# Optimization experiments

Hardware: AMD Instinct MI355X
Metric: run time of the kernel (lower is better)

The kernel has to match this reference:

```python
import jax, jax.numpy as jnp
import numpy as np

B, N, DIM = 2, 2048, 1024
H, DH = 16, 64
INNER = H * DH
LN_EPS = 1e-5
ATTN_EPS = 1e-8
SCALE = DH ** -0.5


def setup_inputs() -> dict:
    key = jax.random.key(0)
    k1, k2, k3 = jax.random.split(key, 3)
    x = jax.random.normal(k1, (B, N, DIM), dtype=jnp.float32)
    ln_gamma = jnp.ones((DIM,), dtype=jnp.float32)
    ln_beta = jnp.zeros((DIM,), dtype=jnp.float32)
    w_qkv = jax.random.normal(k2, (DIM, 3 * INNER), dtype=jnp.float32) * 0.02
    w_out = jax.random.normal(k3, (INNER, DIM), dtype=jnp.float32) * 0.02
    b_out = jnp.zeros((DIM,), dtype=jnp.float32)
    return {"x": x, "ln_gamma": ln_gamma, "ln_beta": ln_beta,
            "w_qkv": w_qkv, "w_out": w_out, "b_out": b_out}


def reference(x, ln_gamma, ln_beta, w_qkv, w_out, b_out):
    # LayerNorm over last dim (biased variance, eps=1e-5)
    mu = jnp.mean(x, axis=-1, keepdims=True)
    var = jnp.var(x, axis=-1, keepdims=True)
    xn = (x - mu) * jax.lax.rsqrt(var + LN_EPS) * ln_gamma + ln_beta
    # QKV projection (no bias), split heads: b n (h d) -> b h n d
    qkv = xn @ w_qkv                                    # [B, N, 3*INNER]
    q, k, v = jnp.split(qkv, 3, axis=-1)
    split_heads = lambda t: t.reshape(B, N, H, DH).transpose(0, 2, 1, 3)
    q, k, v = split_heads(q), split_heads(k), split_heads(v)
    # 'softmax' attn_type: exp(scale * q k^T), normalized by row-sum + eps
    scores = jnp.einsum('bhnd,bhmd->bhnm', q, k) * SCALE   # [B, H, N, N]
    numer = jnp.exp(scores)
    denom = jnp.sum(numer, axis=-1, keepdims=True) + ATTN_EPS
    attn = numer / denom
    out = jnp.einsum('bhnm,bhmd->bhnd', attn, v)           # [B, H, N, DH]
    out = out.transpose(0, 2, 1, 3).reshape(B, N, INNER)   # b h n d -> b n (h d)
    return out @ w_out + b_out
```

## Files before the change

### kernel.cpp

```cpp
#include <hip/hip_runtime.h>
#include <hip/hip_bf16.h>

#define NB    2
#define SEQ   2048
#define DIM_  1024
#define NH    16
#define DHD   64
#define INNER 1024
#define ROWS  4096

typedef _Float16 half_t;
typedef __attribute__((ext_vector_type(4))) _Float16 half4;
typedef __attribute__((ext_vector_type(8))) _Float16 half8;
typedef __attribute__((ext_vector_type(4))) float f32x4;
typedef __attribute__((ext_vector_type(16))) float f32x16;
typedef __attribute__((ext_vector_type(2))) int int2v;
typedef __attribute__((ext_vector_type(4))) int int4v;

__device__ __forceinline__ void async16(const void* g, void* l) {
    __builtin_amdgcn_global_load_lds(
        (const __attribute__((address_space(1))) unsigned int*)g,
        (__attribute__((address_space(3))) unsigned int*)l, 16, 0, 0);
}

__device__ __forceinline__ float ldf(const void* p, size_t i, int isb) {
    if (isb) {
        unsigned int v = ((unsigned int)((const unsigned short*)p)[i]) << 16;
        return __uint_as_float(v);
    }
    return ((const float*)p)[i];
}

__global__ void detect_dtype(const unsigned short* x, int* flag) {
    int tid = threadIdx.x;
    int cnt = 0;
    for (int i = tid; i < 2048; i += 64) {
        float f = __uint_as_float(((unsigned int)x[2 * i]) << 16);
        float a = fabsf(f);
        if (a >= 0.0009765625f && a <= 16.0f) cnt++;
    }
    for (int off = 32; off > 0; off >>= 1) cnt += __shfl_down(cnt, off);
    if (tid == 0) flag[0] = (cnt > 1024) ? 1 : 0;
}

__global__ __launch_bounds__(256) void ln_kernel(const void* __restrict__ x,
                                                 const void* __restrict__ gamma,
                                                 const void* __restrict__ beta,
                                                 half_t* __restrict__ xn,
                                                 const int* __restrict__ flag) {
    int row = blockIdx.x;
    int isb = flag[0];
    int tid = threadIdx.x;
    float vals[4];
    float s = 0.f, ss = 0.f;
    if (!isb) {
        float4 xv = *(const float4*)((const float*)x + (size_t)row * DIM_ + tid * 4);
        vals[0] = xv.x; vals[1] = xv.y; vals[2] = xv.z; vals[3] = xv.w;
    } else {
        #pragma unroll
        for (int j = 0; j < 4; j++) vals[j] = ldf(x, (size_t)row * DIM_ + tid * 4 + j, isb);
    }
    #pragma unroll
    for (int j = 0; j < 4; j++) { s += vals[j]; ss += vals[j] * vals[j]; }
    __shared__ float red[2][4];
    for (int off = 32; off > 0; off >>= 1) {
        s += __shfl_down(s, off);
        ss += __shfl_down(ss, off);
    }
    int wid = tid >> 6;
    if ((tid & 63) == 0) { red[0][wid] = s; red[1][wid] = ss; }
    __syncthreads();
    if (tid == 0) {
        float S = 0.f, SS = 0.f;
        for (int w = 0; w < 4; w++) { S += red[0][w]; SS += red[1][w]; }
        float mu = S / 1024.f;
        float var = SS / 1024.f - mu * mu;
        red[0][0] = mu;
        red[1][0] = rsqrtf(var + 1e-5f);
    }
    __syncthreads();
    float mu = red[0][0], r = red[1][0];
    half4 o;
    #pragma unroll
    for (int j = 0; j < 4; j++) {
        int c = tid * 4 + j;
        float g = ldf(gamma, c, isb);
        float b = ldf(beta, c, isb);
        o[j] = (half_t)((vals[j] - mu) * r * g + b);
    }
    *(half4*)(xn + (size_t)row * DIM_ + tid * 4) = o;
}

__global__ __launch_bounds__(256) void wtrans(const void* __restrict__ W,
                                              half_t* __restrict__ WT,
                                              int K_, int N_,
                                              const int* __restrict__ flag) {
    __shared__ half_t T[64][72];
    int isb = flag[0];
    int k0 = blockIdx.y * 64, n0 = blockIdx.x * 64;
    int t = threadIdx.x;
    if (!isb) {
        #pragma unroll
        for (int p = 0; p < 4; p++) {
            int idx = p * 256 + t;
            int r = idx >> 4, c4 = (idx & 15) * 4;
            float4 xv = *(const float4*)((const float*)W + (size_t)(k0 + r) * N_ + n0 + c4);
            T[r][c4] = (half_t)xv.x; T[r][c4 + 1] = (half_t)xv.y;
            T[r][c4 + 2] = (half_t)xv.z; T[r][c4 + 3] = (half_t)xv.w;
        }
    } else {
        int c = t & 63, rw = t >> 6;
        #pragma unroll
        for (int p = 0; p < 16; p++) {
            int r = p * 4 + rw;
            T[r][c] = (half_t)ldf(W, (size_t)(k0 + r) * N_ + n0 + c, isb);
        }
    }
    __syncthreads();
    int c = t & 63, rw = t >> 6;
    #pragma unroll
    for (int p = 0; p < 16; p++) {
        int r = p * 4 + rw;
        WT[(size_t)(n0 + r) * K_ + k0 + c] = T[c][r];
    }
}

__global__ __launch_bounds__(256) void qkv_gemm(const half_t* __restrict__ A,
                                                const half_t* __restrict__ BT,
                                                half_t* __restrict__ q,
                                                half_t* __restrict__ kp,
                                                half_t* __restrict__ vp) {
    __shared__ half_t As[128 * 64];
    __shared__ half_t Bs[128 * 64];
    int t = threadIdx.x;
    int w = t >> 6, l = t & 63;
    int lm = l & 15, q4 = l >> 4;
    int bid = blockIdx.y * 24 + blockIdx.x;
    int xcd = bid & 7, jj = bid >> 3;
    int r0 = (xcd * 4 + jj / 24) * 128, c0 = (jj % 24) * 128;
    int wr = (w >> 1) * 64, wc = (w & 1) * 64;
    int srow = l >> 3, sg = l & 7;
    f32x4 acc[4][4] = {};
    for (int k0 = 0; k0 < 1024; k0 += 64) {
        __syncthreads();
        #pragma unroll
        for (int p = 0; p < 4; p++) {
            int row = p * 32 + w * 8 + srow;
            int g = sg ^ (srow & 7);
            async16(A + (size_t)(r0 + row) * 1024 + k0 + g * 8, &As[(p * 32 + w * 8) * 64]);
            async16(BT + (size_t)(c0 + row) * 1024 + k0 + g * 8, &Bs[(p * 32 + w * 8) * 64]);
        }
        __syncthreads();
        #pragma unroll
        for (int s = 0; s < 2; s++) {
            half8 av[4], bv[4];
            #pragma unroll
            for (int i = 0; i < 4; i++) {
                int gp = ((s * 4 + q4) ^ (lm & 7)) * 8;
                av[i] = *(const half8*)&As[(wr + i * 16 + lm) * 64 + gp];
                bv[i] = *(const half8*)&Bs[(wc + i * 16 + lm) * 64 + gp];
            }
            #pragma unroll
            for (int i = 0; i < 4; i++)
                #pragma unroll
                for (int j = 0; j < 4; j++)
                    acc[i][j] = __builtin_amdgcn_mfma_f32_16x16x32_f16(bv[j], av[i], acc[i][j], 0, 0, 0);
        }
    }
    #pragma unroll
    for (int i = 0; i < 4; i++) {
        int row = r0 + wr + i * 16 + lm;
        int bb = row >> 11, nn = row & 2047;
        #pragma unroll
        for (int j = 0; j < 4; j++) {
            int f0 = c0 + wc + j * 16 + q4 * 4;
            int which = f0 >> 10, within = f0 & 1023;
            int h = within >> 6, d0 = within & 63;
            int bh = bb * NH + h;
            if (which == 0) {
                half4 val;
                #pragma unroll
                for (int r = 0; r < 4; r++) val[r] = (half_t)acc[i][j][r];
                *(half4*)&q[((size_t)bh * SEQ + nn) * DHD + d0] = val;
            } else if (which == 1) {
                int kt = nn >> 7, kb = (nn >> 5) & 3, qi = nn & 31;
                int ks = d0 >> 4, hf = (d0 >> 3) & 1, e = d0 & 7;
                half4 val;
                #pragma unroll
                for (int r = 0; r < 4; r++) val[r] = (half_t)acc[i][j][r];
                size_t off = ((size_t)bh * 16 + kt) * 8192 +
                             (size_t)(((kb * 4 + ks) * 2 + hf) * 32 + qi) * 8 + e;
                *(half4*)&kp[off] = val;
            } else {
                int kt = nn >> 7, k_in = nn & 127;
                int kb = k_in >> 5, c2 = (k_in >> 4) & 1, rem = k_in & 15;
                int hfv = (rem >> 2) & 1, ev = (rem & 3) | ((rem >> 3) << 2);
                size_t bkt = ((size_t)bh * 16 + kt) * 8192;
                #pragma unroll
                for (int r = 0; r < 4; r++) {
                    int d = d0 + r;
                    int mt2 = d >> 5, qi = d & 31;
                    size_t off = bkt +
                        (size_t)((((kb * 2 + c2) * 2 + mt2) * 64 + hfv * 32 + qi) * 8 + ev);
                    vp[off] = (half_t)acc[i][j][r];
                }
            }
        }
    }
}

__global__ __launch_bounds__(256) void out_gemm(const half_t* __restrict__ A,
                                                const half_t* __restrict__ BT,
                                                const void* __restrict__ bias,
                                                void* __restrict__ outp,
                                                const int* __restrict__ flag) {
    __shared__ half_t As[64 * 64];
    __shared__ half_t Bs[128 * 64];
    int isb = flag[0];
    int t = threadIdx.x;
    int w = t >> 6, l = t & 63;
    int lm = l & 15, q4 = l >> 4;
    int bid = blockIdx.y * 8 + blockIdx.x;
    int xcd = bid & 7, jj = bid >> 3;
    int r0 = (xcd * 8 + jj / 8) * 64, c0 = (jj % 8) * 128;
    int wr = (w >> 1) * 32, wc = (w & 1) * 64;
    int srow = l >> 3, sg = l & 7;
    f32x4 acc[2][4] = {};
    for (int k0 = 0; k0 < 1024; k0 += 64) {
        __syncthreads();
        #pragma unroll
        for (int p = 0; p < 2; p++) {
            int row = p * 32 + w * 8 + srow;
            int g = sg ^ (srow & 7);
            async16(A + (size_t)(r0 + row) * 1024 + k0 + g * 8, &As[(p * 32 + w * 8) * 64]);
        }
        #pragma unroll
        for (int p = 0; p < 4; p++) {
            int row = p * 32 + w * 8 + srow;
            int g = sg ^ (srow & 7);
            async16(BT + (size_t)(c0 + row) * 1024 + k0 + g * 8, &Bs[(p * 32 + w * 8) * 64]);
        }
        __syncthreads();
        #pragma unroll
        for (int s = 0; s < 2; s++) {
            int gp = ((s * 4 + q4) ^ (lm & 7)) * 8;
            half8 av[2], bv[4];
            #pragma unroll
            for (int i = 0; i < 2; i++)
                av[i] = *(const half8*)&As[(wr + i * 16 + lm) * 64 + gp];
            #pragma unroll
            for (int j = 0; j < 4; j++)
                bv[j] = *(const half8*)&Bs[(wc + j * 16 + lm) * 64 + gp];
            #pragma unroll
            for (int i = 0; i < 2; i++)
                #pragma unroll
                for (int j = 0; j < 4; j++)
                    acc[i][j] = __builtin_amdgcn_mfma_f32_16x16x32_f16(bv[j], av[i], acc[i][j], 0, 0, 0);
        }
    }
    #pragma unroll
    for (int i = 0; i < 2; i++) {
        int row = r0 + wr + i * 16 + lm;
        #pragma unroll
        for (int j = 0; j < 4; j++) {
            int col0 = c0 + wc + j * 16 + q4 * 4;
            if (!isb) {
                float4 val;
                float* vpp = (float*)&val;
                #pragma unroll
                for (int r = 0; r < 4; r++)
                    vpp[r] = acc[i][j][r] + ((const float*)bias)[col0 + r];
                *(float4*)&((float*)outp)[(size_t)row * DIM_ + col0] = val;
            } else {
                #pragma unroll
                for (int r = 0; r < 4; r++) {
                    float val = acc[i][j][r] + ldf(bias, col0 + r, isb);
                    ((__hip_bfloat16*)outp)[(size_t)row * DIM_ + col0 + r] = __float2bfloat16(val);
                }
            }
        }
    }
}

__global__ __launch_bounds__(512, 4) void attn_mfma(const half_t* __restrict__ q,
                                                    const half_t* __restrict__ kp,
                                                    const half_t* __restrict__ vp,
                                                    half_t* __restrict__ ao) {
    __shared__ __align__(16) char smem[66048];
    int t = threadIdx.x;
    int w = t >> 6, l = t & 63;
    int qi = l & 31, hf = l >> 5;
    int wq = w & 3, wk = w >> 2;
    int bid = blockIdx.x;
    int xcd = bid & 7, jj = bid >> 3;
    int bh = xcd * 4 + (jj >> 4), qt = jj & 15;
    int b = bh >> 4, hd = bh & 15;
    int qrow = qt * 128 + wq * 32 + qi;

    const char* kpb = (const char*)kp + (size_t)bh * 16 * 16384;
    const char* vpb = (const char*)vp + (size_t)bh * 16 * 16384;

    half8 qf[4];
    #pragma unroll
    for (int ks = 0; ks < 4; ks++) {
        qf[ks] = *(const half8*)(q + ((size_t)bh * SEQ + qrow) * DHD + ks * 16 + hf * 8);
        qf[ks] *= (_Float16)0.125f;
    }

    f32x16 oacc[2] = {};
    float lacc = 0.f;

    #pragma unroll
    for (int r = 0; r < 2; r++) {
        async16(kpb + r * 8192 + w * 1024 + l * 16, smem + r * 8192 + w * 1024);
        async16(vpb + r * 8192 + w * 1024 + l * 16, smem + 16384 + r * 8192 + w * 1024);
    }

    for (int kt = 0; kt < 16; kt++) {
        int cur = kt & 1;
        __syncthreads();
        if (kt < 15) {
            const char* kg = kpb + (size_t)(kt + 1) * 16384;
            const char* vg = vpb + (size_t)(kt + 1) * 16384;
            char* dst = smem + (cur ^ 1) * 32768;
            #pragma unroll
            for (int r = 0; r < 2; r++) {
                async16(kg + r * 8192 + w * 1024 + l * 16, dst + r * 8192 + w * 1024);
                async16(vg + r * 8192 + w * 1024 + l * 16, dst + 16384 + r * 8192 + w * 1024);
            }
        }
        const half_t* Kt = (const half_t*)(smem + cur * 32768);
        const half_t* Vt = (const half_t*)(smem + cur * 32768 + 16384);
        half8 kreg[2][4];
        #pragma unroll
        for (int mt = 0; mt < 2; mt++)
            #pragma unroll
            for (int ks = 0; ks < 4; ks++)
                kreg[mt][ks] = *(const half8*)(Kt + ((wk * 2 + mt) * 4 + ks) * 512 + l * 8);
        half8 vreg[2][2][2];
        #pragma unroll
        for (int mt = 0; mt < 2; mt++)
            #pragma unroll
            for (int c = 0; c < 2; c++)
                #pragma unroll
                for (int mt2 = 0; mt2 < 2; mt2++)
                    vreg[mt][c][mt2] = *(const half8*)(Vt +
                        (((wk * 2 + mt) * 2 + c) * 2 + mt2) * 512 + l * 8);
        #pragma unroll
        for (int mt = 0; mt < 2; mt++) {
            f32x16 sacc = {};
            #pragma unroll
            for (int ks = 0; ks < 4; ks++)
                sacc = __builtin_amdgcn_mfma_f32_32x32x16_f16(kreg[mt][ks], qf[ks], sacc, 0, 0, 0);
            half4 quads[4];
            #pragma unroll
            for (int g = 0; g < 4; g++) {
                #pragma unroll
                for (int s2 = 0; s2 < 4; s2++) {
                    float e = __expf(sacc[g * 4 + s2]);
                    lacc += e;
                    quads[g][s2] = (half_t)e;
                }
            }
            #pragma unroll
            for (int c = 0; c < 2; c++) {
                int2v s0 = __builtin_bit_cast(int2v, quads[2 * c]);
                int2v s1 = __builtin_bit_cast(int2v, quads[2 * c + 1]);
                int4v bi;
                bi.x = s0.x; bi.y = s0.y; bi.z = s1.x; bi.w = s1.y;
                half8 bfrag = __builtin_bit_cast(half8, bi);
                #pragma unroll
                for (int mt2 = 0; mt2 < 2; mt2++)
                    oacc[mt2] = __builtin_amdgcn_mfma_f32_32x32x16_f16(vreg[mt][c][mt2], bfrag, oacc[mt2], 0, 0, 0);
            }
        }
    }
    lacc += __shfl_xor(lacc, 32);

    float* Osh = (float*)smem;
    float* Lsh = (float*)(smem + 65536);
    if (wk == 1) {
        #pragma unroll
        for (int mt2 = 0; mt2 < 2; mt2++)
            #pragma unroll
            for (int reg = 0; reg < 16; reg++) {
                int d = mt2 * 32 + (reg & 3) + 8 * (reg >> 2) + 4 * hf;
                Osh[wq * 2048 + d * 32 + qi] = oacc[mt2][reg];
            }
        if (hf == 0) Lsh[wq * 32 + qi] = lacc;
    }
    __syncthreads();
    if (wk == 0) {
        float ltot = lacc + Lsh[wq * 32 + qi];
        float inv = 1.0f / (ltot + 1e-8f);
        #pragma unroll
        for (int mt2 = 0; mt2 < 2; mt2++)
            #pragma unroll
            for (int r2 = 0; r2 < 4; r2++) {
                int d0 = mt2 * 32 + 8 * r2 + 4 * hf;
                half4 ov;
                #pragma unroll
                for (int r = 0; r < 4; r++) {
                    float vsum = oacc[mt2][r2 * 4 + r] + Osh[wq * 2048 + (d0 + r) * 32 + qi];
                    ov[r] = (_Float16)(vsum * inv);
                }
                *(half4*)(ao + (size_t)(b * SEQ + qrow) * INNER + hd * 64 + d0) = ov;
            }
    }
}

extern "C" void kernel_launch(void* const* d_in, const int* in_sizes, int n_in,
                              void* d_out, int out_size, void* d_ws, size_t ws_size,
                              hipStream_t stream) {
    const void* x     = d_in[0];
    const void* gamma = d_in[1];
    const void* beta  = d_in[2];
    const void* wqkv  = d_in[3];
    const void* wout  = d_in[4];
    const void* bout  = d_in[5];

    char* ws = (char*)d_ws;
    int*    flag   = (int*)ws;
    half_t* xn16   = (half_t*)(ws + 256);
    half_t* wqkvT  = xn16  + (size_t)4096 * 1024;
    half_t* woutT  = wqkvT + (size_t)3072 * 1024;
    half_t* q16    = woutT + (size_t)1024 * 1024;
    half_t* kp16   = q16   + (size_t)4096 * 1024;
    half_t* vp16   = kp16  + (size_t)4096 * 1024;
    half_t* ao16   = vp16  + (size_t)4096 * 1024;

    detect_dtype<<<1, 64, 0, stream>>>((const unsigned short*)x, flag);
    ln_kernel<<<ROWS, 256, 0, stream>>>(x, gamma, beta, xn16, flag);
    wtrans<<<dim3(48, 16), 256, 0, stream>>>(wqkv, wqkvT, 1024, 3072, flag);
    wtrans<<<dim3(16, 16), 256, 0, stream>>>(wout, woutT, 1024, 1024, flag);
    qkv_gemm<<<dim3(24, 32), 256, 0, stream>>>(xn16, wqkvT, q16, kp16, vp16);
    attn_mfma<<<dim3(512), 512, 0, stream>>>(q16, kp16, vp16, ao16);
    out_gemm<<<dim3(8, 64), 256, 0, stream>>>(ao16, woutT, bout, d_out, flag);
}
```

Baseline: 207.3 us.

## Process two query subtiles per warp to reuse K/V fragments in attention

Each attention block now covers 256 query rows instead of 128, and each warp handles two 32-row query subtiles. This lets the K and V fragments loaded from LDS feed twice as many MFMAs, and the grid is halved to 256 blocks. The aim is to cut LDS and global K/V traffic per query row. In exchange register pressure rises (the occupancy hint in launch bounds is dropped), there are fewer blocks to hide latency, and an extra barrier is needed because the output reduction buffer now covers the whole of shared memory.

Result: faster. 202.8 us (-2.2%).

```diff
diff --git a/kernel.cpp b/kernel.cpp
--- a/kernel.cpp
+++ b/kernel.cpp
@@ -282,33 +282,36 @@
     }
 }
 
-__global__ __launch_bounds__(512, 4) void attn_mfma(const half_t* __restrict__ q,
-                                                    const half_t* __restrict__ kp,
-                                                    const half_t* __restrict__ vp,
-                                                    half_t* __restrict__ ao) {
-    __shared__ __align__(16) char smem[66048];
+__global__ __launch_bounds__(512) void attn_mfma(const half_t* __restrict__ q,
+                                                 const half_t* __restrict__ kp,
+                                                 const half_t* __restrict__ vp,
+                                                 half_t* __restrict__ ao) {
+    __shared__ __align__(16) char smem[66560];
     int t = threadIdx.x;
     int w = t >> 6, l = t & 63;
     int qi = l & 31, hf = l >> 5;
     int wq = w & 3, wk = w >> 2;
     int bid = blockIdx.x;
     int xcd = bid & 7, jj = bid >> 3;
-    int bh = xcd * 4 + (jj >> 4), qt = jj & 15;
+    int bh = xcd * 4 + (jj >> 3), qt = jj & 7;
     int b = bh >> 4, hd = bh & 15;
-    int qrow = qt * 128 + wq * 32 + qi;
+    int qrow0 = qt * 256 + wq * 64;
 
     const char* kpb = (const char*)kp + (size_t)bh * 16 * 16384;
     const char* vpb = (const char*)vp + (size_t)bh * 16 * 16384;
 
-    half8 qf[4];
-    #pragma unroll
-    for (int ks = 0; ks < 4; ks++) {
-        qf[ks] = *(const half8*)(q + ((size_t)bh * SEQ + qrow) * DHD + ks * 16 + hf * 8);
-        qf[ks] *= (_Float16)0.125f;
-    }
-
-    f32x16 oacc[2] = {};
-    float lacc = 0.f;
+    half8 qf[2][4];
+    #pragma unroll
+    for (int sq = 0; sq < 2; sq++)
+        #pragma unroll
+        for (int ks = 0; ks < 4; ks++) {
+            qf[sq][ks] = *(const half8*)(q +
+                ((size_t)bh * SEQ + qrow0 + sq * 32 + qi) * DHD + ks * 16 + hf * 8);
+            qf[sq][ks] *= (_Float16)0.125f;
+        }
+
+    f32x16 oacc[2][2] = {};
+    float lacc[2] = {0.f, 0.f};
 
     #pragma unroll
     for (int r = 0; r < 2; r++) {
@@ -348,64 +351,77 @@
                         (((wk * 2 + mt) * 2 + c) * 2 + mt2) * 512 + l * 8);
         #pragma unroll
         for (int mt = 0; mt < 2; mt++) {
-            f32x16 sacc = {};
-            #pragma unroll
-            for (int ks = 0; ks < 4; ks++)
-                sacc = __builtin_amdgcn_mfma_f32_32x32x16_f16(kreg[mt][ks], qf[ks], sacc, 0, 0, 0);
-            half4 quads[4];
-            #pragma unroll
-            for (int g = 0; g < 4; g++) {
-                #pragma unroll
-                for (int s2 = 0; s2 < 4; s2++) {
-                    float e = __expf(sacc[g * 4 + s2]);
-                    lacc += e;
-                    quads[g][s2] = (half_t)e;
+            #pragma unroll
+            for (int sq = 0; sq < 2; sq++) {
+                f32x16 sacc = {};
+                #pragma unroll
+                for (int ks = 0; ks < 4; ks++)
+                    sacc = __builtin_amdgcn_mfma_f32_32x32x16_f16(kreg[mt][ks], qf[sq][ks], sacc, 0, 0, 0);
+                half4 quads[4];
+                #pragma unroll
+                for (int g = 0; g < 4; g++) {
+                    #pragma unroll
+                    for (int s2 = 0; s2 < 4; s2++) {
+                        float e = __expf(sacc[g * 4 + s2]);
+                        lacc[sq] += e;
+                        quads[g][s2] = (half_t)e;
+                    }
+                }
+                #pragma unroll
+                for (int c = 0; c < 2; c++) {
+                    int2v s0 = __builtin_bit_cast(int2v, quads[2 * c]);
+                    int2v s1 = __builtin_bit_cast(int2v, quads[2 * c + 1]);
+                    int4v bi;
+                    bi.x = s0.x; bi.y = s0.y; bi.z = s1.x; bi.w = s1.y;
+                    half8 bfrag = __builtin_bit_cast(half8, bi);
+                    #pragma unroll
+                    for (int mt2 = 0; mt2 < 2; mt2++)
+                        oacc[sq][mt2] = __builtin_amdgcn_mfma_f32_32x32x16_f16(vreg[mt][c][mt2], bfrag, oacc[sq][mt2], 0, 0, 0);
                 }
             }
-            #pragma unroll
-            for (int c = 0; c < 2; c++) {
-                int2v s0 = __builtin_bit_cast(int2v, quads[2 * c]);
-                int2v s1 = __builtin_bit_cast(int2v, quads[2 * c + 1]);
-                int4v bi;
-                bi.x = s0.x; bi.y = s0.y; bi.z = s1.x; bi.w = s1.y;
-                half8 bfrag = __builtin_bit_cast(half8, bi);
-                #pragma unroll
-                for (int mt2 = 0; mt2 < 2; mt2++)
-                    oacc[mt2] = __builtin_amdgcn_mfma_f32_32x32x16_f16(vreg[mt][c][mt2], bfrag, oacc[mt2], 0, 0, 0);
-            }
-        }
-    }
-    lacc += __shfl_xor(lacc, 32);
+        }
+    }
+    lacc[0] += __shfl_xor(lacc[0], 32);
+    lacc[1] += __shfl_xor(lacc[1], 32);
+
+    __syncthreads();
 
     float* Osh = (float*)smem;
     float* Lsh = (float*)(smem + 65536);
     if (wk == 1) {
         #pragma unroll
-        for (int mt2 = 0; mt2 < 2; mt2++)
-            #pragma unroll
-            for (int reg = 0; reg < 16; reg++) {
-                int d = mt2 * 32 + (reg & 3) + 8 * (reg >> 2) + 4 * hf;
-                Osh[wq * 2048 + d * 32 + qi] = oacc[mt2][reg];
-            }
-        if (hf == 0) Lsh[wq * 32 + qi] = lacc;
+        for (int sq = 0; sq < 2; sq++) {
+            #pragma unroll
+            for (int mt2 = 0; mt2 < 2; mt2++)
+                #pragma unroll
+                for (int reg = 0; reg < 16; reg++) {
+                    int d = mt2 * 32 + (reg & 3) + 8 * (reg >> 2) + 4 * hf;
+                    Osh[(wq * 2 + sq) * 2048 + d * 32 + qi] = oacc[sq][mt2][reg];
+                }
+            if (hf == 0) Lsh[(wq * 2 + sq) * 32 + qi] = lacc[sq];
+        }
     }
     __syncthreads();
     if (wk == 0) {
-        float ltot = lacc + Lsh[wq * 32 + qi];
-        float inv = 1.0f / (ltot + 1e-8f);
-        #pragma unroll
-        for (int mt2 = 0; mt2 < 2; mt2++)
-            #pragma unroll
-            for (int r2 = 0; r2 < 4; r2++) {
-                int d0 = mt2 * 32 + 8 * r2 + 4 * hf;
-                half4 ov;
-                #pragma unroll
-                for (int r = 0; r < 4; r++) {
-                    float vsum = oacc[mt2][r2 * 4 + r] + Osh[wq * 2048 + (d0 + r) * 32 + qi];
-                    ov[r] = (_Float16)(vsum * inv);
-                }
-                *(half4*)(ao + (size_t)(b * SEQ + qrow) * INNER + hd * 64 + d0) = ov;
-            }
+        #pragma unroll
+        for (int sq = 0; sq < 2; sq++) {
+            float ltot = lacc[sq] + Lsh[(wq * 2 + sq) * 32 + qi];
+            float inv = 1.0f / (ltot + 1e-8f);
+            #pragma unroll
+            for (int mt2 = 0; mt2 < 2; mt2++)
+                #pragma unroll
+                for (int r2 = 0; r2 < 4; r2++) {
+                    int d0 = mt2 * 32 + 8 * r2 + 4 * hf;
+                    half4 ov;
+                    #pragma unroll
+                    for (int r = 0; r < 4; r++) {
+                        float vsum = oacc[sq][mt2][r2 * 4 + r] +
+                                     Osh[(wq * 2 + sq) * 2048 + (d0 + r) * 32 + qi];
+                        ov[r] = (_Float16)(vsum * inv);
+                    }
+                    *(half4*)(ao + (size_t)(b * SEQ + qrow0 + sq * 32 + qi) * INNER + hd * 64 + d0) = ov;
+                }
+        }
     }
 }
 
@@ -434,6 +450,6 @@
     wtrans<<<dim3(48, 16), 256, 0, stream>>>(wqkv, wqkvT, 1024, 3072, flag);
     wtrans<<<dim3(16, 16), 256, 0, stream>>>(wout, woutT, 1024, 1024, flag);
     qkv_gemm<<<dim3(24, 32), 256, 0, stream>>>(xn16, wqkvT, q16, kp16, vp16);
-    attn_mfma<<<dim3(512), 512, 0, stream>>>(q16, kp16, vp16, ao16);
+    attn_mfma<<<dim3(256), 512, 0, stream>>>(q16, kp16, vp16, ao16);
     out_gemm<<<dim3(8, 64), 256, 0, stream>>>(ao16, woutT, bout, d_out, flag);
 }
```
